# Performance work log

Hardware: AMD Instinct MI355X
Metric: run time of the kernel (lower is better)

Reference implementation:

```python
import jax, jax.numpy as jnp
import numpy as np
import math

NUM_ADCS = 64      # P
NUM_SENSORS = 256  # M
NUM_BLOCKS = 32    # B
BATCH = 4096


def setup_inputs() -> dict:
    key = jax.random.key(0)
    k1, k2 = jax.random.split(key)
    x = jax.random.normal(k1, (BATCH, 2 * NUM_SENSORS * NUM_BLOCKS), dtype=jnp.float32)
    p_values = jax.random.normal(k2, (NUM_ADCS, 1), dtype=jnp.float32)
    return {"x": x, "p_values": p_values}


def reference(x, p_values):
    P, M, B = NUM_ADCS, NUM_SENSORS, NUM_BLOCKS
    m = jnp.arange(M, dtype=x.dtype)                 # [M]
    phi = p_values * m                               # [P, M]
    ang = -phi * (2.0 * math.pi / M)
    A_real = jnp.cos(ang)                            # [P, M]
    A_imag = jnp.sin(ang)                            # [P, M]
    A1 = jnp.concatenate((A_real, A_imag), axis=0)   # [2P, M]
    A2 = jnp.concatenate((-A_imag, A_real), axis=0)  # [2P, M]
    A = jnp.concatenate((A1, A2), axis=1)            # [2P, 2M]
    # block_diag(*[A]*B) @ x.T  ==  per-block matmul on reshaped x
    batch = x.shape[0]
    xb = x.reshape(batch, B, 2 * M)                  # [batch, B, 2M]
    yb = jnp.einsum('pm,bnm->bnp', A, xb)            # [batch, B, 2P]
    return yb.reshape(batch, B * 2 * P)
```

## Files before the change

### kernel.cpp

```cpp
#include <hip/hip_runtime.h>
#include <hip/hip_bf16.h>

#define P_ADC 64
#define M_SEN 256
#define B_BLK 32
#define BATCHN 4096

#define GK 512
#define GN 128
#define GR (BATCHN * B_BLK)

typedef float  f32x4  __attribute__((ext_vector_type(4)));
typedef __bf16 bf16x8 __attribute__((ext_vector_type(8)));
typedef unsigned int u32x4 __attribute__((ext_vector_type(4)));

__global__ void build_w_frags(const float* __restrict__ pv, __bf16* __restrict__ wfrag) {
    int tid = blockIdx.x * blockDim.x + threadIdx.x;
    if (tid >= 8 * 8 * 64) return;
    int lane = tid & 63;
    int f    = (tid >> 6) & 7;
    int t    = tid >> 9;
    int n    = f * 16 + (lane & 15);
    int g    = lane >> 4;
    bool ph  = (n >= 64);
    float pq = pv[n & 63];
    const float step = -0.02454369260617025967f;
    bf16x8 v;
#pragma unroll
    for (int j = 0; j < 8; ++j) {
        int k  = t * 32 + ((j >> 2) << 4) + g * 4 + (j & 3);
        float ang = pq * (float)k * step;
        float s, c;
        sincosf(ang, &s, &c);
        v[j] = (__bf16)(ph ? s : c);
    }
    *(bf16x8*)(wfrag + (size_t)tid * 8) = v;
}

__global__ __launch_bounds__(512, 4) void analog_gemm(const float* __restrict__ X,
                                                      const __bf16* __restrict__ W,
                                                      float* __restrict__ out) {
    __shared__ __bf16 lw[8 * 8 * 64 * 8];

    const int tid = threadIdx.x;

    {
        const f32x4* src = (const f32x4*)W;
        f32x4* dst = (f32x4*)lw;
#pragma unroll
        for (int i = 0; i < 8; ++i)
            dst[i * 512 + tid] = src[i * 512 + tid];
    }
    __syncthreads();

    const int lane = tid & 63;
    const int wave = tid >> 6;
    const int lr   = lane & 15;
    const int g    = lane >> 4;

    const long rowbase = (long)blockIdx.x * 128 + (long)wave * 16;
    const float* xp = X + (rowbase + lr) * (long)GK + g * 4;
    const bf16x8* wp = (const bf16x8*)lw + lane;

    f32x4 acc[8];
#pragma unroll
    for (int f = 0; f < 8; ++f) acc[f] = (f32x4)0.0f;

#pragma unroll
    for (int t = 0; t < 8; ++t) {
        f32x4 xa = *(const f32x4*)(xp + t * 32);
        f32x4 xb = *(const f32x4*)(xp + t * 32 + 16);
        f32x4 xc = *(const f32x4*)(xp + (t + 8) * 32);
        f32x4 xd = *(const f32x4*)(xp + (t + 8) * 32 + 16);

        bf16x8 b0, b1;
#pragma unroll
        for (int j = 0; j < 4; ++j) {
            b0[j] = (__bf16)xa[j];  b0[4 + j] = (__bf16)xb[j];
            b1[j] = (__bf16)xc[j];  b1[4 + j] = (__bf16)xd[j];
        }
        u32x4 u = __builtin_bit_cast(u32x4, b1);
#pragma unroll
        for (int j = 0; j < 4; ++j) u[j] ^= 0x80008000u;
        bf16x8 b1n = __builtin_bit_cast(bf16x8, u);

#pragma unroll
        for (int f = 0; f < 8; ++f) {
            bf16x8 w = wp[(t * 8 + f) * 64];
            acc[f] = __builtin_amdgcn_mfma_f32_16x16x32_bf16(w, b0, acc[f], 0, 0, 0);
            if (f < 4)
                acc[f + 4] = __builtin_amdgcn_mfma_f32_16x16x32_bf16(w, b1, acc[f + 4], 0, 0, 0);
            else
                acc[f - 4] = __builtin_amdgcn_mfma_f32_16x16x32_bf16(w, b1n, acc[f - 4], 0, 0, 0);
        }
    }

    float* op = out + (rowbase + lr) * (long)GN + g * 4;
#pragma unroll
    for (int f = 0; f < 8; ++f)
        __builtin_nontemporal_store(acc[f], (f32x4*)(op + f * 16));
}

extern "C" void kernel_launch(void* const* d_in, const int* in_sizes, int n_in,
                              void* d_out, int out_size, void* d_ws, size_t ws_size,
                              hipStream_t stream) {
    const float* x  = (const float*)d_in[0];
    const float* pv = (const float*)d_in[1];
    float* out      = (float*)d_out;
    __bf16* wfrag   = (__bf16*)d_ws;

    hipLaunchKernelGGL(build_w_frags, dim3(16), dim3(256), 0, stream, pv, wfrag);
    hipLaunchKernelGGL(analog_gemm, dim3(GR / 128), dim3(512), 0, stream, x, wfrag, out);
}
```

Measured before the change: 63.58 us.

## Fuse twiddle-matrix construction into GEMM kernel and process two row tiles per block

Removes the separate build_w_frags launch and has each GEMM block compute its bf16 cos/sin weight fragments directly into LDS with sinpif/cospif. To amortise that per-block trig work, the grid is halved to 512 blocks and each block loops over two 128-row tiles. This saves one kernel launch and the workspace round trip, but every block now recomputes the weights and the grid has half as many blocks.

```diff
diff --git a/kernel.cpp b/kernel.cpp
--- a/kernel.cpp
+++ b/kernel.cpp
@@ -1,55 +1,37 @@
 #include <hip/hip_runtime.h>
 #include <hip/hip_bf16.h>
 
-#define P_ADC 64
-#define M_SEN 256
-#define B_BLK 32
-#define BATCHN 4096
-
 #define GK 512
 #define GN 128
-#define GR (BATCHN * B_BLK)
+#define GRROWS 131072
 
 typedef float  f32x4  __attribute__((ext_vector_type(4)));
 typedef __bf16 bf16x8 __attribute__((ext_vector_type(8)));
 typedef unsigned int u32x4 __attribute__((ext_vector_type(4)));
 
-__global__ void build_w_frags(const float* __restrict__ pv, __bf16* __restrict__ wfrag) {
-    int tid = blockIdx.x * blockDim.x + threadIdx.x;
-    if (tid >= 8 * 8 * 64) return;
-    int lane = tid & 63;
-    int f    = (tid >> 6) & 7;
-    int t    = tid >> 9;
-    int n    = f * 16 + (lane & 15);
-    int g    = lane >> 4;
-    bool ph  = (n >= 64);
-    float pq = pv[n & 63];
-    const float step = -0.02454369260617025967f;
-    bf16x8 v;
-#pragma unroll
-    for (int j = 0; j < 8; ++j) {
-        int k  = t * 32 + ((j >> 2) << 4) + g * 4 + (j & 3);
-        float ang = pq * (float)k * step;
-        float s, c;
-        sincosf(ang, &s, &c);
-        v[j] = (__bf16)(ph ? s : c);
-    }
-    *(bf16x8*)(wfrag + (size_t)tid * 8) = v;
-}
-
-__global__ __launch_bounds__(512, 4) void analog_gemm(const float* __restrict__ X,
-                                                      const __bf16* __restrict__ W,
-                                                      float* __restrict__ out) {
+__global__ __launch_bounds__(512, 4) void analog_fused(const float* __restrict__ X,
+                                                       const float* __restrict__ pv,
+                                                       float* __restrict__ out) {
     __shared__ __bf16 lw[8 * 8 * 64 * 8];
 
     const int tid = threadIdx.x;
 
-    {
-        const f32x4* src = (const f32x4*)W;
-        f32x4* dst = (f32x4*)lw;
 #pragma unroll
-        for (int i = 0; i < 8; ++i)
-            dst[i * 512 + tid] = src[i * 512 + tid];
+    for (int i = 0; i < 8; ++i) {
+        int slot = i * 512 + tid;
+        int sl = slot & 63, sf = (slot >> 6) & 7, st = slot >> 9;
+        int n  = sf * 16 + (sl & 15);
+        int sg = sl >> 4;
+        float pq = pv[n & 63];
+        bool ph  = (n >= 64);
+        bf16x8 v;
+#pragma unroll
+        for (int j = 0; j < 8; ++j) {
+            int k = st * 32 + ((j >> 2) << 4) + sg * 4 + (j & 3);
+            float arg = pq * (float)k * (-0.0078125f);
+            v[j] = (__bf16)(ph ? sinpif(arg) : cospif(arg));
+        }
+        *(bf16x8*)(lw + (size_t)slot * 8) = v;
     }
     __syncthreads();
 
@@ -58,47 +40,51 @@
     const int lr   = lane & 15;
     const int g    = lane >> 4;
 
-    const long rowbase = (long)blockIdx.x * 128 + (long)wave * 16;
-    const float* xp = X + (rowbase + lr) * (long)GK + g * 4;
     const bf16x8* wp = (const bf16x8*)lw + lane;
 
-    f32x4 acc[8];
+#pragma unroll 1
+    for (int s = 0; s < 2; ++s) {
+        const long rowbase = (long)blockIdx.x * 256 + (long)s * 128 + (long)wave * 16;
+        const float* xp = X + (rowbase + lr) * (long)GK + g * 4;
+
+        f32x4 acc[8];
 #pragma unroll
-    for (int f = 0; f < 8; ++f) acc[f] = (f32x4)0.0f;
+        for (int f = 0; f < 8; ++f) acc[f] = (f32x4)0.0f;
 
 #pragma unroll
-    for (int t = 0; t < 8; ++t) {
-        f32x4 xa = *(const f32x4*)(xp + t * 32);
-        f32x4 xb = *(const f32x4*)(xp + t * 32 + 16);
-        f32x4 xc = *(const f32x4*)(xp + (t + 8) * 32);
-        f32x4 xd = *(const f32x4*)(xp + (t + 8) * 32 + 16);
+        for (int t = 0; t < 8; ++t) {
+            f32x4 xa = *(const f32x4*)(xp + t * 32);
+            f32x4 xb = *(const f32x4*)(xp + t * 32 + 16);
+            f32x4 xc = *(const f32x4*)(xp + (t + 8) * 32);
+            f32x4 xd = *(const f32x4*)(xp + (t + 8) * 32 + 16);
 
-        bf16x8 b0, b1;
+            bf16x8 b0, b1;
 #pragma unroll
-        for (int j = 0; j < 4; ++j) {
-            b0[j] = (__bf16)xa[j];  b0[4 + j] = (__bf16)xb[j];
-            b1[j] = (__bf16)xc[j];  b1[4 + j] = (__bf16)xd[j];
-        }
-        u32x4 u = __builtin_bit_cast(u32x4, b1);
+            for (int j = 0; j < 4; ++j) {
+                b0[j] = (__bf16)xa[j];  b0[4 + j] = (__bf16)xb[j];
+                b1[j] = (__bf16)xc[j];  b1[4 + j] = (__bf16)xd[j];
+            }
+            u32x4 u = __builtin_bit_cast(u32x4, b1);
 #pragma unroll
-        for (int j = 0; j < 4; ++j) u[j] ^= 0x80008000u;
-        bf16x8 b1n = __builtin_bit_cast(bf16x8, u);
+            for (int j = 0; j < 4; ++j) u[j] ^= 0x80008000u;
+            bf16x8 b1n = __builtin_bit_cast(bf16x8, u);
 
 #pragma unroll
-        for (int f = 0; f < 8; ++f) {
-            bf16x8 w = wp[(t * 8 + f) * 64];
-            acc[f] = __builtin_amdgcn_mfma_f32_16x16x32_bf16(w, b0, acc[f], 0, 0, 0);
-            if (f < 4)
-                acc[f + 4] = __builtin_amdgcn_mfma_f32_16x16x32_bf16(w, b1, acc[f + 4], 0, 0, 0);
-            else
-                acc[f - 4] = __builtin_amdgcn_mfma_f32_16x16x32_bf16(w, b1n, acc[f - 4], 0, 0, 0);
+            for (int f = 0; f < 8; ++f) {
+                bf16x8 w = wp[(t * 8 + f) * 64];
+                acc[f] = __builtin_amdgcn_mfma_f32_16x16x32_bf16(w, b0, acc[f], 0, 0, 0);
+                if (f < 4)
+                    acc[f + 4] = __builtin_amdgcn_mfma_f32_16x16x32_bf16(w, b1, acc[f + 4], 0, 0, 0);
+                else
+                    acc[f - 4] = __builtin_amdgcn_mfma_f32_16x16x32_bf16(w, b1n, acc[f - 4], 0, 0, 0);
+            }
         }
+
+        float* op = out + (rowbase + lr) * (long)GN + g * 4;
+#pragma unroll
+        for (int f = 0; f < 8; ++f)
+            __builtin_nontemporal_store(acc[f], (f32x4*)(op + f * 16));
     }
-
-    float* op = out + (rowbase + lr) * (long)GN + g * 4;
-#pragma unroll
-    for (int f = 0; f < 8; ++f)
-        __builtin_nontemporal_store(acc[f], (f32x4*)(op + f * 16));
 }
 
 extern "C" void kernel_launch(void* const* d_in, const int* in_sizes, int n_in,
@@ -107,8 +93,6 @@
     const float* x  = (const float*)d_in[0];
     const float* pv = (const float*)d_in[1];
     float* out      = (float*)d_out;
-    __bf16* wfrag   = (__bf16*)d_ws;
 
-    hipLaunchKernelGGL(build_w_frags, dim3(16), dim3(256), 0, stream, pv, wfrag);
-    hipLaunchKernelGGL(analog_gemm, dim3(GR / 128), dim3(512), 0, stream, x, wfrag, out);
+    hipLaunchKernelGGL(analog_fused, dim3(512), dim3(512), 0, stream, x, pv, out);
 }
```

New measurement: 181.7 us. +185.8%, slower.
